# Kernel optimization log

Measured on AMD Instinct MI355X. Metric: run time of the kernel, lower is better.

## Reference

```python
import jax, jax.numpy as jnp
import numpy as np

D_MODEL = 1024
N_HEAD = 16
ATT_DIM = D_MODEL // N_HEAD  # 64
B, S = 8, 2048


def setup_inputs() -> dict:
    key = jax.random.key(0)
    kq, kk, kv, kwq, kwk, kwv = jax.random.split(key, 6)
    # xavier_uniform bound for Linear(hidden_dim -> att_dim)
    bound = float(np.sqrt(6.0 / (D_MODEL + ATT_DIM)))
    return {
        "q": jax.random.normal(kq, (B, S, D_MODEL), dtype=jnp.float32),
        "k": jax.random.normal(kk, (B, S, D_MODEL), dtype=jnp.float32),
        "v": jax.random.normal(kv, (B, S, D_MODEL), dtype=jnp.float32),
        "Wq": jax.random.uniform(kwq, (ATT_DIM, D_MODEL), jnp.float32, -bound, bound),
        "Wk": jax.random.uniform(kwk, (ATT_DIM, D_MODEL), jnp.float32, -bound, bound),
        "Wv": jax.random.uniform(kwv, (ATT_DIM, D_MODEL), jnp.float32, -bound, bound),
    }


def reference(q, k, v, Wq, Wk, Wv):
    # Linear projections (no bias): [B,S,d_model] @ [d_model,att_dim]
    qp = jnp.einsum('bsd,ed->bse', q, Wq)
    kp = jnp.einsum('bsd,ed->bse', k, Wk)
    vp = jnp.einsum('bsd,ed->bse', v, Wv)
    # Scores: note original divides by att_dim (not sqrt)
    scores = jnp.einsum('bqe,bke->bqk', qp, kp) / ATT_DIM
    probs = jax.nn.softmax(scores, axis=-1)  # [B,S,S]
    att = jnp.einsum('bqk,bke->bqe', probs, vp)  # [B,S,att_dim]
    # dropout is identity in eval mode
    return (att, probs)
```

## Files before the change

### kernel.cpp

```cpp
#include <hip/hip_runtime.h>
#include <hip/hip_bf16.h>

#define D_MODEL 1024
#define ATT_DIM 64
#define BATCH 8
#define SEQ 2048
#define MROWS (BATCH * SEQ)

typedef short bf16x8 __attribute__((ext_vector_type(8)));
typedef float f32x4 __attribute__((ext_vector_type(4)));

#define MFMA16(a, b, c) __builtin_amdgcn_mfma_f32_16x16x32_bf16((a), (b), (c), 0, 0, 0)

__device__ inline short f2bf(float f) {
    union { __hip_bfloat16 h; short s; } u;
    u.h = __float2bfloat16(f);
    return u.s;
}

__global__ __launch_bounds__(256) void wcvt_kernel(
    const float* __restrict__ Wq, const float* __restrict__ Wk,
    const float* __restrict__ Wv, short* __restrict__ Wbf)
{
    const int idx = blockIdx.x * 256 + threadIdx.x;
    const int per = ATT_DIM * D_MODEL;
    const int base = idx * 8;
    const int mi = base / per;
    const int off = base - mi * per;
    const float* src = (mi == 0) ? Wq : (mi == 1 ? Wk : Wv);
    const float sc = (mi == 0) ? (1.0f / 64.0f) : 1.0f;
    const float4 a = *reinterpret_cast<const float4*>(src + off);
    const float4 b = *reinterpret_cast<const float4*>(src + off + 4);
    bf16x8 r;
    r[0] = f2bf(a.x * sc); r[1] = f2bf(a.y * sc);
    r[2] = f2bf(a.z * sc); r[3] = f2bf(a.w * sc);
    r[4] = f2bf(b.x * sc); r[5] = f2bf(b.y * sc);
    r[6] = f2bf(b.z * sc); r[7] = f2bf(b.w * sc);
    *reinterpret_cast<bf16x8*>(Wbf + base) = r;
}

__global__ __launch_bounds__(256) void proj_mfma_kernel(
    const float* __restrict__ q, const float* __restrict__ k,
    const float* __restrict__ v, const short* __restrict__ Wbf,
    short* __restrict__ qp, short* __restrict__ kp, short* __restrict__ vpT)
{
    const int mat = blockIdx.y;
    const float* x = (mat == 0) ? q : (mat == 1 ? k : v);
    const short* W = Wbf + mat * ATT_DIM * D_MODEL;

    __shared__ float red[2][16][65];

    const int tid = threadIdx.x;
    const int w = tid >> 6;
    const int l = tid & 63;
    const int lr = l & 15;
    const int g = l >> 4;
    const int wr = w & 1;
    const int kh = w >> 1;

    const int m0 = blockIdx.x * 32 + wr * 16;
    const long arow = (long)(m0 + lr) * D_MODEL;
    const int kbase = kh * 512;

    f32x4 acc[4] = {};

    for (int kt = 0; kt < 512; kt += 128) {
        float4 abuf[8];
        #pragma unroll
        for (int c = 0; c < 4; ++c) {
            abuf[c * 2]     = *reinterpret_cast<const float4*>(x + arow + kbase + kt + c * 32 + g * 8);
            abuf[c * 2 + 1] = *reinterpret_cast<const float4*>(x + arow + kbase + kt + c * 32 + g * 8 + 4);
        }
        #pragma unroll
        for (int c = 0; c < 4; ++c) {
            bf16x8 af;
            af[0] = f2bf(abuf[c * 2].x);     af[1] = f2bf(abuf[c * 2].y);
            af[2] = f2bf(abuf[c * 2].z);     af[3] = f2bf(abuf[c * 2].w);
            af[4] = f2bf(abuf[c * 2 + 1].x); af[5] = f2bf(abuf[c * 2 + 1].y);
            af[6] = f2bf(abuf[c * 2 + 1].z); af[7] = f2bf(abuf[c * 2 + 1].w);
            #pragma unroll
            for (int ef = 0; ef < 4; ++ef) {
                const bf16x8 bf_ = *reinterpret_cast<const bf16x8*>(
                    W + (ef * 16 + lr) * D_MODEL + kbase + kt + c * 32 + g * 8);
                acc[ef] = MFMA16(af, bf_, acc[ef]);
            }
        }
    }

    if (kh == 1) {
        #pragma unroll
        for (int ef = 0; ef < 4; ++ef)
            #pragma unroll
            for (int j = 0; j < 4; ++j)
                red[wr][g * 4 + j][ef * 16 + lr] = acc[ef][j];
    }
    __syncthreads();
    if (kh == 1) return;

    #pragma unroll
    for (int ef = 0; ef < 4; ++ef)
        #pragma unroll
        for (int j = 0; j < 4; ++j)
            acc[ef][j] += red[wr][g * 4 + j][ef * 16 + lr];

    if (mat < 2) {
        short* out = (mat == 0) ? qp : kp;
        #pragma unroll
        for (int ef = 0; ef < 4; ++ef)
            #pragma unroll
            for (int j = 0; j < 4; ++j)
                out[(long)(m0 + g * 4 + j) * ATT_DIM + ef * 16 + lr] = f2bf(acc[ef][j]);
    } else {
        const int b = m0 / SEQ;
        const int s0 = m0 - b * SEQ;
        #pragma unroll
        for (int ef = 0; ef < 4; ++ef)
            #pragma unroll
            for (int j = 0; j < 4; ++j)
                vpT[((long)b * ATT_DIM + ef * 16 + lr) * SEQ + s0 + g * 4 + j] =
                    f2bf(acc[ef][j]);
    }
}

union AttnSmem {
    struct {
        short p[8][16][40];
        float m[8][16];
        float l[8][16];
    } a;
    float o[8][64][17];
};

__global__ __launch_bounds__(512) void attn_kernel(
    const short* __restrict__ qp, const short* __restrict__ kp,
    const short* __restrict__ vpT, float* __restrict__ probs,
    float* __restrict__ att)
{
    __shared__ AttnSmem lds;

    const int tid = threadIdx.x;
    const int w = tid >> 6;
    const int l = tid & 63;
    const int lr = l & 15;
    const int g = l >> 4;

    const int b = blockIdx.y;
    const int q0 = blockIdx.x * 16;

    const short* qpb = qp + ((long)b * SEQ + q0) * ATT_DIM;
    const short* kpb = kp + (long)b * SEQ * ATT_DIM;
    const short* vTb = vpT + (long)b * ATT_DIM * SEQ;

    const bf16x8 qa0 = *reinterpret_cast<const bf16x8*>(qpb + lr * ATT_DIM + g * 8);
    const bf16x8 qa1 = *reinterpret_cast<const bf16x8*>(qpb + lr * ATT_DIM + 32 + g * 8);

    const int kbeg = w * 256;

    f32x4 s[8][2];
    #pragma unroll
    for (int ch = 0; ch < 8; ++ch) {
        const short* kb = kpb + (long)(kbeg + ch * 32) * ATT_DIM;
        const bf16x8 kb00 = *reinterpret_cast<const bf16x8*>(kb + lr * ATT_DIM + g * 8);
        const bf16x8 kb01 = *reinterpret_cast<const bf16x8*>(kb + lr * ATT_DIM + 32 + g * 8);
        const bf16x8 kb10 = *reinterpret_cast<const bf16x8*>(kb + (16 + lr) * ATT_DIM + g * 8);
        const bf16x8 kb11 = *reinterpret_cast<const bf16x8*>(kb + (16 + lr) * ATT_DIM + 32 + g * 8);
        f32x4 t0 = {}; t0 = MFMA16(qa0, kb00, t0); t0 = MFMA16(qa1, kb01, t0);
        f32x4 t1 = {}; t1 = MFMA16(qa0, kb10, t1); t1 = MFMA16(qa1, kb11, t1);
        s[ch][0] = t0; s[ch][1] = t1;
    }

    float gm[4];
    #pragma unroll
    for (int j = 0; j < 4; ++j) {
        const float m0_ = fmaxf(fmaxf(s[0][0][j], s[0][1][j]), fmaxf(s[1][0][j], s[1][1][j]));
        const float m1_ = fmaxf(fmaxf(s[2][0][j], s[2][1][j]), fmaxf(s[3][0][j], s[3][1][j]));
        const float m2_ = fmaxf(fmaxf(s[4][0][j], s[4][1][j]), fmaxf(s[5][0][j], s[5][1][j]));
        const float m3_ = fmaxf(fmaxf(s[6][0][j], s[6][1][j]), fmaxf(s[7][0][j], s[7][1][j]));
        float mj = fmaxf(fmaxf(m0_, m1_), fmaxf(m2_, m3_));
        mj = fmaxf(mj, __shfl_xor(mj, 1));
        mj = fmaxf(mj, __shfl_xor(mj, 2));
        mj = fmaxf(mj, __shfl_xor(mj, 4));
        mj = fmaxf(mj, __shfl_xor(mj, 8));
        gm[j] = mj;
    }
    if (lr == 0) {
        #pragma unroll
        for (int j = 0; j < 4; ++j) lds.a.m[w][g * 4 + j] = gm[j];
    }
    __syncthreads();
    #pragma unroll
    for (int j = 0; j < 4; ++j) {
        const int qr = g * 4 + j;
        float mf = lds.a.m[0][qr];
        #pragma unroll
        for (int ww = 1; ww < 8; ++ww) mf = fmaxf(mf, lds.a.m[ww][qr]);
        gm[j] = mf;
    }

    float lsum[4] = {0.f, 0.f, 0.f, 0.f};
    #pragma unroll
    for (int ch = 0; ch < 8; ++ch)
        #pragma unroll
        for (int h = 0; h < 2; ++h)
            #pragma unroll
            for (int j = 0; j < 4; ++j) {
                const float e = __expf(s[ch][h][j] - gm[j]);
                s[ch][h][j] = e;
                lsum[j] += e;
            }
    #pragma unroll
    for (int j = 0; j < 4; ++j) {
        float lj = lsum[j];
        lj += __shfl_xor(lj, 1);
        lj += __shfl_xor(lj, 2);
        lj += __shfl_xor(lj, 4);
        lj += __shfl_xor(lj, 8);
        lsum[j] = lj;
    }
    if (lr == 0) {
        #pragma unroll
        for (int j = 0; j < 4; ++j) lds.a.l[w][g * 4 + j] = lsum[j];
    }
    __syncthreads();
    float invl[4];
    #pragma unroll
    for (int j = 0; j < 4; ++j) {
        const int qr = g * 4 + j;
        float lf = lds.a.l[0][qr];
        #pragma unroll
        for (int ww = 1; ww < 8; ++ww) lf += lds.a.l[ww][qr];
        invl[j] = 1.0f / lf;
    }

    f32x4 accO[4] = {};
    float* pbase = probs + ((long)b * SEQ + q0) * SEQ;

    #pragma unroll
    for (int ch = 0; ch < 8; ++ch) {
        const int k0 = kbeg + ch * 32;
        #pragma unroll
        for (int h = 0; h < 2; ++h)
            #pragma unroll
            for (int j = 0; j < 4; ++j) {
                const int qr = g * 4 + j;
                const float p = s[ch][h][j] * invl[j];
                pbase[(long)qr * SEQ + k0 + h * 16 + lr] = p;
                lds.a.p[w][qr][h * 16 + lr] = f2bf(p);
            }
        const bf16x8 pb = *reinterpret_cast<const bf16x8*>(&lds.a.p[w][lr][g * 8]);
        #pragma unroll
        for (int ef = 0; ef < 4; ++ef) {
            const bf16x8 va = *reinterpret_cast<const bf16x8*>(
                vTb + (long)(ef * 16 + lr) * SEQ + k0 + g * 8);
            accO[ef] = MFMA16(va, pb, accO[ef]);
        }
    }

    __syncthreads();
    #pragma unroll
    for (int ef = 0; ef < 4; ++ef)
        #pragma unroll
        for (int j = 0; j < 4; ++j)
            lds.o[w][ef * 16 + g * 4 + j][lr] = accO[ef][j];
    __syncthreads();

    {
        const int qr = tid >> 5;
        const int e0 = (tid & 31) * 2;
        float o0 = 0.f, o1 = 0.f;
        #pragma unroll
        for (int ww = 0; ww < 8; ++ww) {
            o0 += lds.o[ww][e0][qr];
            o1 += lds.o[ww][e0 + 1][qr];
        }
        float2 o = make_float2(o0, o1);
        *reinterpret_cast<float2*>(att + ((long)b * SEQ + q0 + qr) * ATT_DIM + e0) = o;
    }
}

extern "C" void kernel_launch(void* const* d_in, const int* in_sizes, int n_in,
                              void* d_out, int out_size, void* d_ws, size_t ws_size,
                              hipStream_t stream)
{
    const float* q  = (const float*)d_in[0];
    const float* k  = (const float*)d_in[1];
    const float* v  = (const float*)d_in[2];
    const float* Wq = (const float*)d_in[3];
    const float* Wk = (const float*)d_in[4];
    const float* Wv = (const float*)d_in[5];

    float* att   = (float*)d_out;
    float* probs = att + (size_t)BATCH * SEQ * ATT_DIM;

    short* qp  = (short*)d_ws;
    short* kp  = qp + (size_t)MROWS * ATT_DIM;
    short* vpT = kp + (size_t)MROWS * ATT_DIM;
    short* Wbf = vpT + (size_t)MROWS * ATT_DIM;

    wcvt_kernel<<<dim3(96), 256, 0, stream>>>(Wq, Wk, Wv, Wbf);

    proj_mfma_kernel<<<dim3(MROWS / 32, 3), 256, 0, stream>>>(
        q, k, v, Wbf, qp, kp, vpT);

    attn_kernel<<<dim3(SEQ / 16, BATCH), 512, 0, stream>>>(
        qp, kp, vpT, probs, att);
}
```

Baseline: 170.8 us.

## Stage projection input tiles through LDS with async double-buffered global loads

The projection kernel now loads fp32 input rows into double-buffered LDS using direct global-to-LDS loads, with an XOR swizzle to avoid bank conflicts. Each wave owns 16 full rows over the whole K dimension, so the split-K reduction through shared memory is gone, and each block covers 64 rows instead of 32. This is meant to overlap input streaming with MFMA work and hide global memory latency in a bandwidth-bound projection. In exchange it adds a barrier per K step and halves the number of blocks.

After: 151.6 us. 11.2% less time.

```diff
diff --git a/kernel.cpp b/kernel.cpp
--- a/kernel.cpp
+++ b/kernel.cpp
@@ -16,6 +16,12 @@
     union { __hip_bfloat16 h; short s; } u;
     u.h = __float2bfloat16(f);
     return u.s;
+}
+
+__device__ __forceinline__ void gload_lds16(const float* g, float* l) {
+    __builtin_amdgcn_global_load_lds(
+        (const __attribute__((address_space(1))) void*)g,
+        (__attribute__((address_space(3))) void*)l, 16, 0, 0);
 }
 
 __global__ __launch_bounds__(256) void wcvt_kernel(
@@ -48,60 +54,59 @@
     const float* x = (mat == 0) ? q : (mat == 1 ? k : v);
     const short* W = Wbf + mat * ATT_DIM * D_MODEL;
 
-    __shared__ float red[2][16][65];
+    __shared__ float As[2][4096];
 
     const int tid = threadIdx.x;
     const int w = tid >> 6;
     const int l = tid & 63;
     const int lr = l & 15;
     const int g = l >> 4;
-    const int wr = w & 1;
-    const int kh = w >> 1;
-
-    const int m0 = blockIdx.x * 32 + wr * 16;
-    const long arow = (long)(m0 + lr) * D_MODEL;
-    const int kbase = kh * 512;
+
+    const int m0 = blockIdx.x * 64;
+    const int row = w * 16 + lr;
+    const int xr = (row & 7) << 4;
 
     f32x4 acc[4] = {};
 
-    for (int kt = 0; kt < 512; kt += 128) {
-        float4 abuf[8];
-        #pragma unroll
-        for (int c = 0; c < 4; ++c) {
-            abuf[c * 2]     = *reinterpret_cast<const float4*>(x + arow + kbase + kt + c * 32 + g * 8);
-            abuf[c * 2 + 1] = *reinterpret_cast<const float4*>(x + arow + kbase + kt + c * 32 + g * 8 + 4);
+    #define STAGE(c, buf)                                                      \
+        {                                                                      \
+            const int kt_ = (c) * 64;                                          \
+            _Pragma("unroll")                                                  \
+            for (int j = 0; j < 4; ++j) {                                      \
+                const int rs = (w * 4 + j) * 4 + g;                            \
+                const int scb = (lr * 16) ^ ((rs & 7) << 4);                   \
+                gload_lds16(x + (long)(m0 + rs) * D_MODEL + kt_ + (scb >> 2),  \
+                            &As[buf][(w * 4 + j) * 256]);                      \
+            }                                                                  \
         }
-        #pragma unroll
-        for (int c = 0; c < 4; ++c) {
+
+    STAGE(0, 0);
+    __syncthreads();
+
+    for (int c = 0; c < 16; ++c) {
+        const int buf = c & 1;
+        if (c < 15) STAGE(c + 1, buf ^ 1);
+
+        const int kt = c * 64;
+        const char* Ab = (const char*)&As[buf][0] + row * 256;
+        #pragma unroll
+        for (int ks = 0; ks < 2; ++ks) {
+            const int b0 = ks * 128 + g * 32;
+            const float4 a0 = *reinterpret_cast<const float4*>(Ab + (b0 ^ xr));
+            const float4 a1 = *reinterpret_cast<const float4*>(Ab + ((b0 + 16) ^ xr));
             bf16x8 af;
-            af[0] = f2bf(abuf[c * 2].x);     af[1] = f2bf(abuf[c * 2].y);
-            af[2] = f2bf(abuf[c * 2].z);     af[3] = f2bf(abuf[c * 2].w);
-            af[4] = f2bf(abuf[c * 2 + 1].x); af[5] = f2bf(abuf[c * 2 + 1].y);
-            af[6] = f2bf(abuf[c * 2 + 1].z); af[7] = f2bf(abuf[c * 2 + 1].w);
+            af[0] = f2bf(a0.x); af[1] = f2bf(a0.y); af[2] = f2bf(a0.z); af[3] = f2bf(a0.w);
+            af[4] = f2bf(a1.x); af[5] = f2bf(a1.y); af[6] = f2bf(a1.z); af[7] = f2bf(a1.w);
             #pragma unroll
             for (int ef = 0; ef < 4; ++ef) {
-                const bf16x8 bf_ = *reinterpret_cast<const bf16x8*>(
-                    W + (ef * 16 + lr) * D_MODEL + kbase + kt + c * 32 + g * 8);
-                acc[ef] = MFMA16(af, bf_, acc[ef]);
+                const bf16x8 wf = *reinterpret_cast<const bf16x8*>(
+                    W + (ef * 16 + lr) * D_MODEL + kt + ks * 32 + g * 8);
+                acc[ef] = MFMA16(af, wf, acc[ef]);
             }
         }
-    }
-
-    if (kh == 1) {
-        #pragma unroll
-        for (int ef = 0; ef < 4; ++ef)
-            #pragma unroll
-            for (int j = 0; j < 4; ++j)
-                red[wr][g * 4 + j][ef * 16 + lr] = acc[ef][j];
-    }
-    __syncthreads();
-    if (kh == 1) return;
-
-    #pragma unroll
-    for (int ef = 0; ef < 4; ++ef)
-        #pragma unroll
-        for (int j = 0; j < 4; ++j)
-            acc[ef][j] += red[wr][g * 4 + j][ef * 16 + lr];
+        __syncthreads();
+    }
+    #undef STAGE
 
     if (mat < 2) {
         short* out = (mat == 0) ? qp : kp;
@@ -109,10 +114,11 @@
         for (int ef = 0; ef < 4; ++ef)
             #pragma unroll
             for (int j = 0; j < 4; ++j)
-                out[(long)(m0 + g * 4 + j) * ATT_DIM + ef * 16 + lr] = f2bf(acc[ef][j]);
+                out[(long)(m0 + w * 16 + g * 4 + j) * ATT_DIM + ef * 16 + lr] =
+                    f2bf(acc[ef][j]);
     } else {
         const int b = m0 / SEQ;
-        const int s0 = m0 - b * SEQ;
+        const int s0 = (m0 - b * SEQ) + w * 16;
         #pragma unroll
         for (int ef = 0; ef < 4; ++ef)
             #pragma unroll
@@ -299,7 +305,7 @@
 
     wcvt_kernel<<<dim3(96), 256, 0, stream>>>(Wq, Wk, Wv, Wbf);
 
-    proj_mfma_kernel<<<dim3(MROWS / 32, 3), 256, 0, stream>>>(
+    proj_mfma_kernel<<<dim3(MROWS / 64, 3), 256, 0, stream>>>(
         q, k, v, Wbf, qp, kp, vpT);
 
     attn_kernel<<<dim3(SEQ / 16, BATCH), 512, 0, stream>>>(
```
